# Performance work log

Hardware: AMD Instinct MI355X
Metric: run time of the kernel (lower is better)

## Reference

```python
import jax, jax.numpy as jnp
import numpy as np

S = 16        # neighbor samples per layer
NL = 2        # number of GNN layers


def setup_inputs() -> dict:
    key = jax.random.key(0)
    ks = jax.random.split(key, 12)
    N_NODES, D, E, NMP, DEG, N_EDGE, B, NC = 50000, 128, 32, 3, 32, 200000, 1024, 8
    sc = 0.05
    return {
        "ids": jax.random.randint(ks[0], (B,), 0, N_NODES, dtype=jnp.int32),
        "feats": jax.random.normal(ks[1], (N_NODES, D), jnp.float32),
        "edge_emb": jax.random.normal(ks[2], (NMP, N_EDGE, E), jnp.float32),
        "adj_nodes": jax.random.randint(ks[3], (NMP, N_NODES, DEG), 0, N_NODES, dtype=jnp.int32),
        "adj_edges": jax.random.randint(ks[4], (NMP, N_NODES, DEG), 0, N_EDGE, dtype=jnp.int32),
        "W_self": jax.random.normal(ks[5], (NMP, NL, D, D), jnp.float32) * sc,
        "W_neigh": jax.random.normal(ks[6], (NMP, NL, D + E, D), jnp.float32) * sc,
        "W_edge": jax.random.normal(ks[7], (NMP, NL, 2 * D + E, E), jnp.float32) * sc,
        "attn": jax.random.normal(ks[8], (D,), jnp.float32) * sc,
        "fc_w": jax.random.normal(ks[9], (D, NC), jnp.float32) * sc,
        "fc_b": jnp.zeros((NC,), jnp.float32),
    }


def reference(ids, feats, edge_emb, adj_nodes, adj_edges, W_self, W_neigh, W_edge, attn, fc_w, fc_b):
    NMP = adj_nodes.shape[0]
    outs = []
    for mp in range(NMP):
        # --- sample neighbor tree (deterministic: first S columns) ---
        cur = ids
        all_feats = [feats[cur]]
        all_edges = []
        for _ in range(NL):
            nb = adj_nodes[mp][cur][:, :S].reshape(-1)     # [N*S]
            eid = adj_edges[mp][cur][:, :S].reshape(-1)    # [N*S]
            all_edges.append(edge_emb[mp][eid])            # [N*S, E]
            cur = nb
            all_feats.append(feats[cur])
        # --- per-layer aggregation + edge update ---
        for l in range(NL):
            new_feats = []
            for k in range(len(all_feats) - 1):
                xs, xn, ee = all_feats[k], all_feats[k + 1], all_edges[k]
                N = xs.shape[0]
                # mean over sampled neighbors of [neigh_feat || edge_emb]
                nin = jnp.concatenate(
                    [xn.reshape(N, S, -1), ee.reshape(N, S, -1)], axis=-1
                ).mean(axis=1)                             # [N, D+E]
                new_feats.append(jax.nn.relu(xs @ W_self[mp, l] + nin @ W_neigh[mp, l]))
            all_feats = new_feats  # dropout is identity in eval mode
            new_edges = []
            for k in range(len(all_edges) - 1):
                xs, xn, ee = all_feats[k], all_feats[k + 1], all_edges[k]
                rep = jnp.repeat(xs, S, axis=0)            # [N*S, D]
                new_edges.append(jax.nn.relu(
                    jnp.concatenate([rep, xn, ee], axis=-1) @ W_edge[mp, l]))
            all_edges = new_edges
        outs.append(all_feats[0])                          # [B, D]
    stacked = jnp.stack(outs)                              # [NMP, B, D]
    # metapath attention fuse
    scores = jnp.tanh(jnp.einsum('mbd,d->mb', stacked, attn))
    beta = jax.nn.softmax(scores, axis=0)
    emb = jnp.einsum('mb,mbd->bd', beta, stacked)          # [B, D]
    # F.normalize(dim=1)
    emb = emb / jnp.maximum(jnp.linalg.norm(emb, axis=1, keepdims=True), 1e-12)
    return emb @ fc_w + fc_b
```

## Files before the change

kernel.cpp:

```cpp
#include <hip/hip_runtime.h>

#define NNODES  50000
#define D       128
#define E       32
#define NMP     3
#define DEG     32
#define NEDGE   200000
#define B       1024
#define NC      8
#define S       16

#define RPM      17408
#define NKT      9
#define WSTRIDE  36864
#define WESTRIDE 9216

#define CONV_TASKS (1600000 + 6 * WSTRIDE + 3 * WESTRIDE)
#define TOT_TASKS  (CONV_TASKS + 3 * RPM)

typedef float f4 __attribute__((ext_vector_type(4)));
typedef short bh8 __attribute__((ext_vector_type(8)));

static __device__ __forceinline__ unsigned short f2bf(float f) {
    unsigned int u = __float_as_uint(f);
    u = u + 0x7FFFu + ((u >> 16) & 1u);
    return (unsigned short)(u >> 16);
}
static __device__ __forceinline__ float bf2f(unsigned short h) {
    return __uint_as_float(((unsigned int)h) << 16);
}

__global__ __launch_bounds__(256) void convsamp_k(
    const float* __restrict__ feats, const float* __restrict__ Ws,
    const float* __restrict__ Wn, const float* __restrict__ We,
    const int* __restrict__ ids, const int* __restrict__ adjn,
    const int* __restrict__ adje,
    unsigned short* __restrict__ fb, unsigned short* __restrict__ WT0,
    unsigned short* __restrict__ WTe, int* __restrict__ gx, int* __restrict__ eid1)
{
    int i = blockIdx.x * 256 + threadIdx.x;
    if (i < 1600000) {
        float4 v = ((const float4*)feats)[i];
        unsigned int p0 = (unsigned int)f2bf(v.x) | ((unsigned int)f2bf(v.y) << 16);
        unsigned int p1 = (unsigned int)f2bf(v.z) | ((unsigned int)f2bf(v.w) << 16);
        ((uint2*)fb)[i] = make_uint2(p0, p1);
    } else if (i < 1600000 + 6 * WSTRIDE) {
        int i2 = i - 1600000;
        int ml = i2 / WSTRIDE, e = i2 % WSTRIDE;
        int j = e & 7, t1 = e >> 3;
        int n = t1 & 127, t2 = t1 >> 7;
        int q = t2 & 3, kt = t2 >> 2;
        int k = kt * 32 + q * 8 + j;
        float v = (k < 128) ? Ws[((size_t)ml * 128 + k) * 128 + n]
                            : Wn[((size_t)ml * 160 + (k - 128)) * 128 + n];
        WT0[(size_t)ml * WSTRIDE + e] = f2bf(v);
    } else if (i < CONV_TASKS) {
        int i3 = i - 1600000 - 6 * WSTRIDE;
        int mp = i3 / WESTRIDE, e = i3 % WESTRIDE;
        int j = e & 7, t1 = e >> 3;
        int n = t1 & 31, t2 = t1 >> 5;
        int q = t2 & 3, kt = t2 >> 2;
        int k = kt * 32 + q * 8 + j;
        float v = We[(((size_t)mp * 2) * 288 + k) * 32 + n];
        WTe[(size_t)mp * WESTRIDE + e] = f2bf(v);
    } else if (i < TOT_TASKS) {
        int i4 = i - CONV_TASKS;
        int mp = i4 / RPM, r = i4 % RPM;
        if (r < 16384) {
            int node = ids[r >> 4];
            gx[mp * RPM + r]     = adjn[((size_t)mp * NNODES + node) * DEG + (r & 15)];
            eid1[mp * 16384 + r] = adje[((size_t)mp * NNODES + node) * DEG + (r & 15)];
        } else {
            gx[mp * RPM + r] = ids[r - 16384];
        }
    }
}

__global__ __launch_bounds__(256) void aggfeat_k(
    const unsigned short* __restrict__ fb, const float* __restrict__ edge_emb,
    const int* __restrict__ adjn, const int* __restrict__ adje,
    const int* __restrict__ gx, const int* __restrict__ eid1,
    const unsigned short* __restrict__ WT0,
    unsigned short* __restrict__ fout)
{
    __shared__ unsigned short Asm[16][136];
    __shared__ unsigned short Nsm[16][168];
    const int mp = blockIdx.y;
    const int w = threadIdx.x >> 6, t = threadIdx.x & 63;
    const int r0 = blockIdx.x * 16;
    const float* ee = edge_emb + (size_t)mp * NEDGE * E;
    const int hi = t >> 5, t31 = t & 31;
    const float inv = 1.0f / (float)S;
    const unsigned int* fb32 = (const unsigned int*)fb;
    const int lvl1 = (r0 < 16384);

    for (int pp = 0; pp < 2; ++pp) {
        const int lra = w * 4 + pp * 2, lrb = lra + 1;
        const int ra = r0 + lra, rb = r0 + lrb;
        const int sa = __builtin_amdgcn_readfirstlane(gx[mp * RPM + ra]);
        const int sb = __builtin_amdgcn_readfirstlane(gx[mp * RPM + rb]);
        const int *ipa, *eixa, *ipb, *eixb;
        if (lvl1) {
            ipa  = adjn + ((size_t)mp * NNODES + sa) * DEG;
            eixa = adje + ((size_t)mp * NNODES + sa) * DEG;
            ipb  = adjn + ((size_t)mp * NNODES + sb) * DEG;
            eixb = adje + ((size_t)mp * NNODES + sb) * DEG;
        } else {
            ipa  = gx + mp * RPM + (ra - 16384) * S;
            eixa = eid1 + mp * 16384 + (ra - 16384) * S;
            ipb  = gx + mp * RPM + (rb - 16384) * S;
            eixb = eid1 + mp * 16384 + (rb - 16384) * S;
        }
        unsigned int ava = fb32[(size_t)sa * 64 + t];
        unsigned int avb = fb32[(size_t)sb * 64 + t];
        unsigned int fva[S], fvb[S];
#pragma unroll
        for (int j = 0; j < S; ++j) {
            int na = __builtin_amdgcn_readfirstlane(ipa[j]);
            fva[j] = fb32[(size_t)na * 64 + t];
        }
#pragma unroll
        for (int j = 0; j < S; ++j) {
            int nb = __builtin_amdgcn_readfirstlane(ipb[j]);
            fvb[j] = fb32[(size_t)nb * 64 + t];
        }
        float eva[S / 2], evb[S / 2];
#pragma unroll
        for (int e = 0; e < S / 2; ++e) {
            int a_ev = __builtin_amdgcn_readfirstlane(eixa[2 * e]);
            int a_od = __builtin_amdgcn_readfirstlane(eixa[2 * e + 1]);
            eva[e] = ee[(size_t)(hi ? a_od : a_ev) * E + t31];
        }
#pragma unroll
        for (int e = 0; e < S / 2; ++e) {
            int b_ev = __builtin_amdgcn_readfirstlane(eixb[2 * e]);
            int b_od = __builtin_amdgcn_readfirstlane(eixb[2 * e + 1]);
            evb[e] = ee[(size_t)(hi ? b_od : b_ev) * E + t31];
        }

        float sa0 = 0.f, sa1 = 0.f, sea = 0.f;
        float sb0 = 0.f, sb1 = 0.f, seb = 0.f;
#pragma unroll
        for (int j = 0; j < S; ++j) {
            sa0 += bf2f((unsigned short)(fva[j] & 0xFFFF));
            sa1 += bf2f((unsigned short)(fva[j] >> 16));
            sb0 += bf2f((unsigned short)(fvb[j] & 0xFFFF));
            sb1 += bf2f((unsigned short)(fvb[j] >> 16));
        }
#pragma unroll
        for (int e = 0; e < S / 2; ++e) { sea += eva[e]; seb += evb[e]; }
        sea += __shfl_xor(sea, 32);
        seb += __shfl_xor(seb, 32);

        ((unsigned int*)&Asm[lra][0])[t] = ava;
        ((unsigned int*)&Asm[lrb][0])[t] = avb;
        ((unsigned int*)&Nsm[lra][0])[t] =
            (unsigned int)f2bf(sa0 * inv) | ((unsigned int)f2bf(sa1 * inv) << 16);
        ((unsigned int*)&Nsm[lrb][0])[t] =
            (unsigned int)f2bf(sb0 * inv) | ((unsigned int)f2bf(sb1 * inv) << 16);
        if (t < E) {
            Nsm[lra][128 + t] = f2bf(sea * inv);
            Nsm[lrb][128 + t] = f2bf(seb * inv);
        }
    }
    __syncthreads();

    const int q = t >> 4, lm = t & 15;
    const unsigned short* wb = WT0 + (size_t)mp * 2 * WSTRIDE;

    f4 acc[2];
    acc[0] = (f4){0.f, 0.f, 0.f, 0.f};
    acc[1] = (f4){0.f, 0.f, 0.f, 0.f};

#pragma unroll
    for (int kt = 0; kt < NKT; ++kt) {
        const int k0 = kt * 32 + q * 8;
        bh8 a = (k0 < 128) ? *(const bh8*)&Asm[lm][k0]
                           : *(const bh8*)&Nsm[lm][k0 - 128];
        const unsigned short* wrow = wb + ((size_t)(kt * 4 + q) * 128 + lm) * 8;
#pragma unroll
        for (int ntl = 0; ntl < 2; ++ntl) {
            bh8 bf = *(const bh8*)(wrow + (w * 2 + ntl) * 16 * 8);
            acc[ntl] = __builtin_amdgcn_mfma_f32_16x16x32_bf16(a, bf, acc[ntl], 0, 0, 0);
        }
    }

#pragma unroll
    for (int ntl = 0; ntl < 2; ++ntl)
#pragma unroll
        for (int rr = 0; rr < 4; ++rr) {
            int row = r0 + q * 4 + rr;
            int col = (w * 2 + ntl) * 16 + lm;
            fout[((size_t)mp * RPM + row) * 128 + col] = f2bf(fmaxf(acc[ntl][rr], 0.f));
        }
}

__global__ __launch_bounds__(256) void edgeagg_k(
    const unsigned short* __restrict__ fout, const float* __restrict__ edge_emb,
    const int* __restrict__ eid1, const unsigned short* __restrict__ WTe,
    unsigned short* __restrict__ agg1)
{
    const int mp = blockIdx.y;
    const int w = threadIdx.x >> 6, l = threadIdx.x & 63;
    const int q = l >> 4, lm = l & 15;
    const int m0 = blockIdx.x * 128 + w * 32;
    const unsigned short* we = WTe + (size_t)mp * WESTRIDE;
    const unsigned short* f1base = fout + (size_t)mp * RPM * 128;
    const unsigned short* f0base = fout + ((size_t)mp * RPM + 16384) * 128;
    const float* ee = edge_emb + (size_t)mp * NEDGE * E;
    const float inv = 1.0f / (float)S;

    const unsigned short* a1p[2];
    const unsigned short* a0p[2];
    int eidL[2];
#pragma unroll
    for (int mt = 0; mt < 2; ++mt) {
        int row = m0 + mt * 16 + lm;
        a1p[mt] = f1base + (size_t)row * 128;
        a0p[mt] = f0base + (size_t)(row >> 4) * 128;
        eidL[mt] = eid1[mp * 16384 + row];
    }

    f4 acc[2][2];
#pragma unroll
    for (int mt = 0; mt < 2; ++mt) { acc[mt][0] = (f4){0,0,0,0}; acc[mt][1] = (f4){0,0,0,0}; }

#pragma unroll
    for (int kt = 0; kt < NKT; ++kt) {
        const int k0 = kt * 32 + q * 8;
        bh8 a[2];
#pragma unroll
        for (int mt = 0; mt < 2; ++mt) {
            if (kt < 4) {
                a[mt] = *(const bh8*)(a0p[mt] + k0);
            } else if (kt < 8) {
                a[mt] = *(const bh8*)(a1p[mt] + (k0 - 128));
            } else {
                const float* ep = ee + (size_t)eidL[mt] * E + q * 8;
                float4 v0 = *(const float4*)ep;
                float4 v1 = *(const float4*)(ep + 4);
                bh8 tv;
                tv[0] = (short)f2bf(v0.x); tv[1] = (short)f2bf(v0.y);
                tv[2] = (short)f2bf(v0.z); tv[3] = (short)f2bf(v0.w);
                tv[4] = (short)f2bf(v1.x); tv[5] = (short)f2bf(v1.y);
                tv[6] = (short)f2bf(v1.z); tv[7] = (short)f2bf(v1.w);
                a[mt] = tv;
            }
        }
        const unsigned short* wrow = we + ((size_t)(kt * 4 + q) * 32 + lm) * 8;
        bh8 b0 = *(const bh8*)(wrow);
        bh8 b1 = *(const bh8*)(wrow + 16 * 8);
#pragma unroll
        for (int mt = 0; mt < 2; ++mt) {
            acc[mt][0] = __builtin_amdgcn_mfma_f32_16x16x32_bf16(a[mt], b0, acc[mt][0], 0, 0, 0);
            acc[mt][1] = __builtin_amdgcn_mfma_f32_16x16x32_bf16(a[mt], b1, acc[mt][1], 0, 0, 0);
        }
    }

#pragma unroll
    for (int mt = 0; mt < 2; ++mt) {
        int seg = (m0 >> 4) + mt;
#pragma unroll
        for (int nt = 0; nt < 2; ++nt) {
            float ps = 0.f;
#pragma unroll
            for (int rr = 0; rr < 4; ++rr) ps += fmaxf(acc[mt][nt][rr], 0.f);
            ps += __shfl_xor(ps, 16);
            ps += __shfl_xor(ps, 32);
            if (l < 16)
                agg1[((size_t)mp * B + seg) * 160 + 128 + nt * 16 + lm] = f2bf(ps * inv);
        }
    }

#pragma unroll
    for (int mt = 0; mt < 2; ++mt) {
        int seg = (m0 >> 4) + mt;
        const unsigned short* fr = f1base + (size_t)seg * 16 * 128;
        float s0 = 0.f, s1 = 0.f;
#pragma unroll
        for (int j = 0; j < S; ++j) {
            unsigned int u = ((const unsigned int*)(fr + j * 128))[l];
            s0 += bf2f((unsigned short)(u & 0xFFFF));
            s1 += bf2f((unsigned short)(u >> 16));
        }
        ((unsigned int*)(agg1 + ((size_t)mp * B + seg) * 160))[l] =
            (unsigned int)f2bf(s0 * inv) | ((unsigned int)f2bf(s1 * inv) << 16);
    }
}

__global__ __launch_bounds__(256) void feat1fin_k(
    const unsigned short* __restrict__ fout, const unsigned short* __restrict__ agg1,
    const unsigned short* __restrict__ WT0,
    const float* __restrict__ attn, const float* __restrict__ fcw,
    const float* __restrict__ fcb, float* __restrict__ out)
{
    __shared__ float sbuf[NMP][32][132];
    const int w = threadIdx.x >> 6, l = threadIdx.x & 63;
    const int q = l >> 4, lm = l & 15;
    const int m0 = blockIdx.x * 32;

    for (int task = w; task < 6; task += 4) {
        const int mp = task >> 1, mt = task & 1;
        const int row = m0 + mt * 16 + lm;
        const unsigned short* ap = fout + ((size_t)mp * RPM + 16384 + row) * 128;
        const unsigned short* np = agg1 + ((size_t)mp * B + row) * 160;
        const unsigned short* wb = WT0 + ((size_t)mp * 2 + 1) * WSTRIDE;

        f4 acc[8];
#pragma unroll
        for (int nt = 0; nt < 8; ++nt) acc[nt] = (f4){0.f, 0.f, 0.f, 0.f};
#pragma unroll
        for (int kt = 0; kt < NKT; ++kt) {
            const int k0 = kt * 32 + q * 8;
            bh8 a = (k0 < 128) ? *(const bh8*)(ap + k0) : *(const bh8*)(np + (k0 - 128));
            const unsigned short* wrow = wb + ((size_t)(kt * 4 + q) * 128 + lm) * 8;
#pragma unroll
            for (int nt = 0; nt < 8; ++nt) {
                bh8 bf = *(const bh8*)(wrow + nt * 16 * 8);
                acc[nt] = __builtin_amdgcn_mfma_f32_16x16x32_bf16(a, bf, acc[nt], 0, 0, 0);
            }
        }
#pragma unroll
        for (int nt = 0; nt < 8; ++nt)
#pragma unroll
            for (int rr = 0; rr < 4; ++rr)
                sbuf[mp][mt * 16 + q * 4 + rr][nt * 16 + lm] = fmaxf(acc[nt][rr], 0.f);
    }
    __syncthreads();

    const int row = threadIdx.x >> 3;
    const int j = threadIdx.x & 7;
    const int d0 = j * 16;
    float sc[NMP];
#pragma unroll
    for (int mp = 0; mp < NMP; ++mp) {
        float p = 0.f;
#pragma unroll
        for (int d = 0; d < 16; ++d) p += sbuf[mp][row][d0 + d] * attn[d0 + d];
        p += __shfl_xor(p, 1); p += __shfl_xor(p, 2); p += __shfl_xor(p, 4);
        sc[mp] = tanhf(p);
    }
    float mx = fmaxf(sc[0], fmaxf(sc[1], sc[2]));
    float e0 = expf(sc[0] - mx), e1 = expf(sc[1] - mx), e2 = expf(sc[2] - mx);
    float isum = 1.f / (e0 + e1 + e2);
    float b0 = e0 * isum, b1 = e1 * isum, b2 = e2 * isum;

    float emb[16];
    float nn = 0.f;
#pragma unroll
    for (int d = 0; d < 16; ++d) {
        float v = b0 * sbuf[0][row][d0 + d] + b1 * sbuf[1][row][d0 + d]
                + b2 * sbuf[2][row][d0 + d];
        emb[d] = v;
        nn += v * v;
    }
    nn += __shfl_xor(nn, 1); nn += __shfl_xor(nn, 2); nn += __shfl_xor(nn, 4);
    float innorm = 1.f / fmaxf(sqrtf(nn), 1e-12f);
#pragma unroll
    for (int d = 0; d < 16; ++d) emb[d] *= innorm;

#pragma unroll
    for (int c = 0; c < NC; ++c) {
        float p = 0.f;
#pragma unroll
        for (int d = 0; d < 16; ++d) p += emb[d] * fcw[(d0 + d) * NC + c];
        p += __shfl_xor(p, 1); p += __shfl_xor(p, 2); p += __shfl_xor(p, 4);
        if (j == c) out[(size_t)(m0 + row) * NC + c] = p + fcb[c];
    }
}

extern "C" void kernel_launch(void* const* d_in, const int* in_sizes, int n_in,
                              void* d_out, int out_size, void* d_ws, size_t ws_size,
                              hipStream_t stream) {
    const int* ids        = (const int*)d_in[0];
    const float* feats    = (const float*)d_in[1];
    const float* edge_emb = (const float*)d_in[2];
    const int* adjn       = (const int*)d_in[3];
    const int* adje       = (const int*)d_in[4];
    const float* Ws       = (const float*)d_in[5];
    const float* Wn       = (const float*)d_in[6];
    const float* We       = (const float*)d_in[7];
    const float* attn     = (const float*)d_in[8];
    const float* fcw      = (const float*)d_in[9];
    const float* fcb      = (const float*)d_in[10];
    float* out = (float*)d_out;

    char* p = (char*)d_ws;
    unsigned short* WT0 = (unsigned short*)p; p += (size_t)6 * WSTRIDE * 2;
    unsigned short* WTe = (unsigned short*)p; p += (size_t)3 * WESTRIDE * 2;
    unsigned short* fb  = (unsigned short*)p; p += (size_t)NNODES * 128 * 2;
    int* gx   = (int*)p;                      p += (size_t)3 * RPM * 4;
    int* eid1 = (int*)p;                      p += (size_t)3 * 16384 * 4;
    unsigned short* fout = (unsigned short*)p; p += (size_t)3 * RPM * 128 * 2;
    unsigned short* agg1 = (unsigned short*)p; p += (size_t)3 * B * 160 * 2;

    convsamp_k<<<TOT_TASKS / 256, 256, 0, stream>>>(feats, Ws, Wn, We, ids, adjn, adje,
                                                    fb, WT0, WTe, gx, eid1);
    aggfeat_k<<<dim3(RPM / 16, 3), 256, 0, stream>>>(fb, edge_emb, adjn, adje, gx, eid1,
                                                     WT0, fout);
    edgeagg_k<<<dim3(128, 3), 256, 0, stream>>>(fout, edge_emb, eid1, WTe, agg1);
    feat1fin_k<<<32, 256, 0, stream>>>(fout, agg1, WT0, attn, fcw, fcb, out);
}
```

Measured before the change: 243.3 us.

## Vectorize neighbor gathers in aggfeat and split edge and final kernels into more blocks

aggfeat_k now preloads each row's neighbor and edge indices straight from the adjacency arrays as vectors, one slice per lane group, instead of using scalar readfirstlane index loads. Feature rows are gathered as 16-byte loads per lane and edge embeddings as float4, and partial sums are combined with cross-lane shuffles. The separate level-0 and level-1 index paths become one, and a launch_bounds occupancy hint is added. edgeagg_k and feat1fin_k handle half as many rows per block and launch twice as many blocks to spread work over more CUs. The cost is extra shuffle reductions and more redundant weight loads per block.

```diff
diff --git a/kernel.cpp b/kernel.cpp
--- a/kernel.cpp
+++ b/kernel.cpp
@@ -20,6 +20,10 @@
 
 typedef float f4 __attribute__((ext_vector_type(4)));
 typedef short bh8 __attribute__((ext_vector_type(8)));
+typedef unsigned int uv4 __attribute__((ext_vector_type(4)));
+typedef unsigned int uv2 __attribute__((ext_vector_type(2)));
+typedef int iv4 __attribute__((ext_vector_type(4)));
+typedef int iv2 __attribute__((ext_vector_type(2)));
 
 static __device__ __forceinline__ unsigned short f2bf(float f) {
     unsigned int u = __float_as_uint(f);
@@ -76,7 +80,7 @@
     }
 }
 
-__global__ __launch_bounds__(256) void aggfeat_k(
+__global__ __launch_bounds__(256, 4) void aggfeat_k(
     const unsigned short* __restrict__ fb, const float* __restrict__ edge_emb,
     const int* __restrict__ adjn, const int* __restrict__ adje,
     const int* __restrict__ gx, const int* __restrict__ eid1,
@@ -86,86 +90,106 @@
     __shared__ unsigned short Asm[16][136];
     __shared__ unsigned short Nsm[16][168];
     const int mp = blockIdx.y;
-    const int w = threadIdx.x >> 6, t = threadIdx.x & 63;
+    const int w = threadIdx.x >> 6, l = threadIdx.x & 63;
     const int r0 = blockIdx.x * 16;
+    const unsigned int* fb32 = (const unsigned int*)fb;
     const float* ee = edge_emb + (size_t)mp * NEDGE * E;
-    const int hi = t >> 5, t31 = t & 31;
     const float inv = 1.0f / (float)S;
-    const unsigned int* fb32 = (const unsigned int*)fb;
-    const int lvl1 = (r0 < 16384);
-
+    const int g = l >> 4, c = l & 15;
+    const int d8 = l & 7;
+
+    int srcs[4];
+#pragma unroll
+    for (int rr = 0; rr < 4; ++rr)
+        srcs[rr] = gx[mp * RPM + r0 + w * 4 + rr];
+
+    iv4 nIdx[4]; iv2 eIdx[4]; unsigned int selfu[4];
+#pragma unroll
+    for (int rr = 0; rr < 4; ++rr) {
+        const int* nb = adjn + ((size_t)mp * NNODES + srcs[rr]) * DEG;
+        const int* eb = adje + ((size_t)mp * NNODES + srcs[rr]) * DEG;
+        nIdx[rr] = *(const iv4*)(nb + 4 * g);
+        eIdx[rr] = *(const iv2*)(eb + 2 * (l >> 3));
+        selfu[rr] = fb32[(size_t)srcs[rr] * 64 + l];
+    }
+
+#pragma unroll
     for (int pp = 0; pp < 2; ++pp) {
-        const int lra = w * 4 + pp * 2, lrb = lra + 1;
-        const int ra = r0 + lra, rb = r0 + lrb;
-        const int sa = __builtin_amdgcn_readfirstlane(gx[mp * RPM + ra]);
-        const int sb = __builtin_amdgcn_readfirstlane(gx[mp * RPM + rb]);
-        const int *ipa, *eixa, *ipb, *eixb;
-        if (lvl1) {
-            ipa  = adjn + ((size_t)mp * NNODES + sa) * DEG;
-            eixa = adje + ((size_t)mp * NNODES + sa) * DEG;
-            ipb  = adjn + ((size_t)mp * NNODES + sb) * DEG;
-            eixb = adje + ((size_t)mp * NNODES + sb) * DEG;
-        } else {
-            ipa  = gx + mp * RPM + (ra - 16384) * S;
-            eixa = eid1 + mp * 16384 + (ra - 16384) * S;
-            ipb  = gx + mp * RPM + (rb - 16384) * S;
-            eixb = eid1 + mp * 16384 + (rb - 16384) * S;
-        }
-        unsigned int ava = fb32[(size_t)sa * 64 + t];
-        unsigned int avb = fb32[(size_t)sb * 64 + t];
-        unsigned int fva[S], fvb[S];
-#pragma unroll
-        for (int j = 0; j < S; ++j) {
-            int na = __builtin_amdgcn_readfirstlane(ipa[j]);
-            fva[j] = fb32[(size_t)na * 64 + t];
-        }
-#pragma unroll
-        for (int j = 0; j < S; ++j) {
-            int nb = __builtin_amdgcn_readfirstlane(ipb[j]);
-            fvb[j] = fb32[(size_t)nb * 64 + t];
-        }
-        float eva[S / 2], evb[S / 2];
-#pragma unroll
-        for (int e = 0; e < S / 2; ++e) {
-            int a_ev = __builtin_amdgcn_readfirstlane(eixa[2 * e]);
-            int a_od = __builtin_amdgcn_readfirstlane(eixa[2 * e + 1]);
-            eva[e] = ee[(size_t)(hi ? a_od : a_ev) * E + t31];
-        }
-#pragma unroll
-        for (int e = 0; e < S / 2; ++e) {
-            int b_ev = __builtin_amdgcn_readfirstlane(eixb[2 * e]);
-            int b_od = __builtin_amdgcn_readfirstlane(eixb[2 * e + 1]);
-            evb[e] = ee[(size_t)(hi ? b_od : b_ev) * E + t31];
-        }
-
-        float sa0 = 0.f, sa1 = 0.f, sea = 0.f;
-        float sb0 = 0.f, sb1 = 0.f, seb = 0.f;
-#pragma unroll
-        for (int j = 0; j < S; ++j) {
-            sa0 += bf2f((unsigned short)(fva[j] & 0xFFFF));
-            sa1 += bf2f((unsigned short)(fva[j] >> 16));
-            sb0 += bf2f((unsigned short)(fvb[j] & 0xFFFF));
-            sb1 += bf2f((unsigned short)(fvb[j] >> 16));
-        }
-#pragma unroll
-        for (int e = 0; e < S / 2; ++e) { sea += eva[e]; seb += evb[e]; }
-        sea += __shfl_xor(sea, 32);
-        seb += __shfl_xor(seb, 32);
-
-        ((unsigned int*)&Asm[lra][0])[t] = ava;
-        ((unsigned int*)&Asm[lrb][0])[t] = avb;
-        ((unsigned int*)&Nsm[lra][0])[t] =
-            (unsigned int)f2bf(sa0 * inv) | ((unsigned int)f2bf(sa1 * inv) << 16);
-        ((unsigned int*)&Nsm[lrb][0])[t] =
-            (unsigned int)f2bf(sb0 * inv) | ((unsigned int)f2bf(sb1 * inv) << 16);
-        if (t < E) {
-            Nsm[lra][128 + t] = f2bf(sea * inv);
-            Nsm[lrb][128 + t] = f2bf(seb * inv);
+        const int lra = w * 4 + 2 * pp, lrb = lra + 1;
+        const int ia = 2 * pp, ib = 2 * pp + 1;
+
+        uv4 gA[4], gB[4];
+#pragma unroll
+        for (int p = 0; p < 4; ++p)
+            gA[p] = *(const uv4*)(fb32 + (size_t)nIdx[ia][p] * 64 + c * 4);
+#pragma unroll
+        for (int p = 0; p < 4; ++p)
+            gB[p] = *(const uv4*)(fb32 + (size_t)nIdx[ib][p] * 64 + c * 4);
+        f4 eA0 = *(const f4*)(ee + (size_t)eIdx[ia][0] * E + d8 * 4);
+        f4 eA1 = *(const f4*)(ee + (size_t)eIdx[ia][1] * E + d8 * 4);
+        f4 eB0 = *(const f4*)(ee + (size_t)eIdx[ib][0] * E + d8 * 4);
+        f4 eB1 = *(const f4*)(ee + (size_t)eIdx[ib][1] * E + d8 * 4);
+
+        float accA[8], accB[8];
+#pragma unroll
+        for (int d = 0; d < 8; ++d) { accA[d] = 0.f; accB[d] = 0.f; }
+#pragma unroll
+        for (int p = 0; p < 4; ++p)
+#pragma unroll
+            for (int qq = 0; qq < 4; ++qq) {
+                unsigned int ua = gA[p][qq], ub = gB[p][qq];
+                accA[2 * qq]     += __uint_as_float(ua << 16);
+                accA[2 * qq + 1] += __uint_as_float(ua & 0xffff0000u);
+                accB[2 * qq]     += __uint_as_float(ub << 16);
+                accB[2 * qq + 1] += __uint_as_float(ub & 0xffff0000u);
+            }
+#pragma unroll
+        for (int d = 0; d < 8; ++d) {
+            accA[d] += __shfl_xor(accA[d], 16);
+            accA[d] += __shfl_xor(accA[d], 32);
+            accB[d] += __shfl_xor(accB[d], 16);
+            accB[d] += __shfl_xor(accB[d], 32);
+        }
+        float feA[4], feB[4];
+#pragma unroll
+        for (int qq = 0; qq < 4; ++qq) {
+            feA[qq] = eA0[qq] + eA1[qq];
+            feB[qq] = eB0[qq] + eB1[qq];
+            feA[qq] += __shfl_xor(feA[qq], 8);
+            feA[qq] += __shfl_xor(feA[qq], 16);
+            feA[qq] += __shfl_xor(feA[qq], 32);
+            feB[qq] += __shfl_xor(feB[qq], 8);
+            feB[qq] += __shfl_xor(feB[qq], 16);
+            feB[qq] += __shfl_xor(feB[qq], 32);
+        }
+
+        ((unsigned int*)&Asm[lra][0])[l] = selfu[ia];
+        ((unsigned int*)&Asm[lrb][0])[l] = selfu[ib];
+        if (g == 0) {
+            uv4 oa, ob;
+#pragma unroll
+            for (int qq = 0; qq < 4; ++qq) {
+                oa[qq] = (unsigned int)f2bf(accA[2 * qq] * inv)
+                       | ((unsigned int)f2bf(accA[2 * qq + 1] * inv) << 16);
+                ob[qq] = (unsigned int)f2bf(accB[2 * qq] * inv)
+                       | ((unsigned int)f2bf(accB[2 * qq + 1] * inv) << 16);
+            }
+            *(uv4*)&Nsm[lra][c * 8] = oa;
+            *(uv4*)&Nsm[lrb][c * 8] = ob;
+        }
+        if (l < 8) {
+            uv2 oa, ob;
+            oa[0] = (unsigned int)f2bf(feA[0] * inv) | ((unsigned int)f2bf(feA[1] * inv) << 16);
+            oa[1] = (unsigned int)f2bf(feA[2] * inv) | ((unsigned int)f2bf(feA[3] * inv) << 16);
+            ob[0] = (unsigned int)f2bf(feB[0] * inv) | ((unsigned int)f2bf(feB[1] * inv) << 16);
+            ob[1] = (unsigned int)f2bf(feB[2] * inv) | ((unsigned int)f2bf(feB[3] * inv) << 16);
+            *(uv2*)&Nsm[lra][128 + d8 * 4] = oa;
+            *(uv2*)&Nsm[lrb][128 + d8 * 4] = ob;
         }
     }
     __syncthreads();
 
-    const int q = t >> 4, lm = t & 15;
+    const int q = l >> 4, lm = l & 15;
     const unsigned short* wb = WT0 + (size_t)mp * 2 * WSTRIDE;
 
     f4 acc[2];
@@ -203,78 +227,61 @@
     const int mp = blockIdx.y;
     const int w = threadIdx.x >> 6, l = threadIdx.x & 63;
     const int q = l >> 4, lm = l & 15;
-    const int m0 = blockIdx.x * 128 + w * 32;
+    const int m0 = blockIdx.x * 64 + w * 16;
     const unsigned short* we = WTe + (size_t)mp * WESTRIDE;
     const unsigned short* f1base = fout + (size_t)mp * RPM * 128;
     const unsigned short* f0base = fout + ((size_t)mp * RPM + 16384) * 128;
     const float* ee = edge_emb + (size_t)mp * NEDGE * E;
     const float inv = 1.0f / (float)S;
 
-    const unsigned short* a1p[2];
-    const unsigned short* a0p[2];
-    int eidL[2];
-#pragma unroll
-    for (int mt = 0; mt < 2; ++mt) {
-        int row = m0 + mt * 16 + lm;
-        a1p[mt] = f1base + (size_t)row * 128;
-        a0p[mt] = f0base + (size_t)(row >> 4) * 128;
-        eidL[mt] = eid1[mp * 16384 + row];
-    }
-
-    f4 acc[2][2];
-#pragma unroll
-    for (int mt = 0; mt < 2; ++mt) { acc[mt][0] = (f4){0,0,0,0}; acc[mt][1] = (f4){0,0,0,0}; }
+    const int row = m0 + lm;
+    const unsigned short* a1p = f1base + (size_t)row * 128;
+    const unsigned short* a0p = f0base + (size_t)(row >> 4) * 128;
+    const int eidL = eid1[mp * 16384 + row];
+
+    f4 acc[2];
+    acc[0] = (f4){0.f, 0.f, 0.f, 0.f};
+    acc[1] = (f4){0.f, 0.f, 0.f, 0.f};
 
 #pragma unroll
     for (int kt = 0; kt < NKT; ++kt) {
         const int k0 = kt * 32 + q * 8;
-        bh8 a[2];
-#pragma unroll
-        for (int mt = 0; mt < 2; ++mt) {
-            if (kt < 4) {
-                a[mt] = *(const bh8*)(a0p[mt] + k0);
-            } else if (kt < 8) {
-                a[mt] = *(const bh8*)(a1p[mt] + (k0 - 128));
-            } else {
-                const float* ep = ee + (size_t)eidL[mt] * E + q * 8;
-                float4 v0 = *(const float4*)ep;
-                float4 v1 = *(const float4*)(ep + 4);
-                bh8 tv;
-                tv[0] = (short)f2bf(v0.x); tv[1] = (short)f2bf(v0.y);
-                tv[2] = (short)f2bf(v0.z); tv[3] = (short)f2bf(v0.w);
-                tv[4] = (short)f2bf(v1.x); tv[5] = (short)f2bf(v1.y);
-                tv[6] = (short)f2bf(v1.z); tv[7] = (short)f2bf(v1.w);
-                a[mt] = tv;
-            }
+        bh8 a;
+        if (kt < 4) {
+            a = *(const bh8*)(a0p + k0);
+        } else if (kt < 8) {
+            a = *(const bh8*)(a1p + (k0 - 128));
+        } else {
+            const float* ep = ee + (size_t)eidL * E + q * 8;
+            float4 v0 = *(const float4*)ep;
+            float4 v1 = *(const float4*)(ep + 4);
+            bh8 tv;
+            tv[0] = (short)f2bf(v0.x); tv[1] = (short)f2bf(v0.y);
+            tv[2] = (short)f2bf(v0.z); tv[3] = (short)f2bf(v0.w);
+            tv[4] = (short)f2bf(v1.x); tv[5] = (short)f2bf(v1.y);
+            tv[6] = (short)f2bf(v1.z); tv[7] = (short)f2bf(v1.w);
+            a = tv;
         }
         const unsigned short* wrow = we + ((size_t)(kt * 4 + q) * 32 + lm) * 8;
         bh8 b0 = *(const bh8*)(wrow);
         bh8 b1 = *(const bh8*)(wrow + 16 * 8);
-#pragma unroll
-        for (int mt = 0; mt < 2; ++mt) {
-            acc[mt][0] = __builtin_amdgcn_mfma_f32_16x16x32_bf16(a[mt], b0, acc[mt][0], 0, 0, 0);
-            acc[mt][1] = __builtin_amdgcn_mfma_f32_16x16x32_bf16(a[mt], b1, acc[mt][1], 0, 0, 0);
-        }
-    }
-
-#pragma unroll
-    for (int mt = 0; mt < 2; ++mt) {
-        int seg = (m0 >> 4) + mt;
-#pragma unroll
-        for (int nt = 0; nt < 2; ++nt) {
-            float ps = 0.f;
-#pragma unroll
-            for (int rr = 0; rr < 4; ++rr) ps += fmaxf(acc[mt][nt][rr], 0.f);
-            ps += __shfl_xor(ps, 16);
-            ps += __shfl_xor(ps, 32);
-            if (l < 16)
-                agg1[((size_t)mp * B + seg) * 160 + 128 + nt * 16 + lm] = f2bf(ps * inv);
-        }
-    }
-
-#pragma unroll
-    for (int mt = 0; mt < 2; ++mt) {
-        int seg = (m0 >> 4) + mt;
+        acc[0] = __builtin_amdgcn_mfma_f32_16x16x32_bf16(a, b0, acc[0], 0, 0, 0);
+        acc[1] = __builtin_amdgcn_mfma_f32_16x16x32_bf16(a, b1, acc[1], 0, 0, 0);
+    }
+
+    const int seg = m0 >> 4;
+#pragma unroll
+    for (int nt = 0; nt < 2; ++nt) {
+        float ps = 0.f;
+#pragma unroll
+        for (int rr = 0; rr < 4; ++rr) ps += fmaxf(acc[nt][rr], 0.f);
+        ps += __shfl_xor(ps, 16);
+        ps += __shfl_xor(ps, 32);
+        if (l < 16)
+            agg1[((size_t)mp * B + seg) * 160 + 128 + nt * 16 + lm] = f2bf(ps * inv);
+    }
+
+    {
         const unsigned short* fr = f1base + (size_t)seg * 16 * 128;
         float s0 = 0.f, s1 = 0.f;
 #pragma unroll
@@ -294,78 +301,80 @@
     const float* __restrict__ attn, const float* __restrict__ fcw,
     const float* __restrict__ fcb, float* __restrict__ out)
 {
-    __shared__ float sbuf[NMP][32][132];
+    __shared__ float sbuf[NMP][16][132];
     const int w = threadIdx.x >> 6, l = threadIdx.x & 63;
     const int q = l >> 4, lm = l & 15;
-    const int m0 = blockIdx.x * 32;
+    const int m0 = blockIdx.x * 16;
 
     for (int task = w; task < 6; task += 4) {
-        const int mp = task >> 1, mt = task & 1;
-        const int row = m0 + mt * 16 + lm;
+        const int mp = task >> 1, nh = task & 1;
+        const int row = m0 + lm;
         const unsigned short* ap = fout + ((size_t)mp * RPM + 16384 + row) * 128;
         const unsigned short* np = agg1 + ((size_t)mp * B + row) * 160;
         const unsigned short* wb = WT0 + ((size_t)mp * 2 + 1) * WSTRIDE;
 
-        f4 acc[8];
-#pragma unroll
-        for (int nt = 0; nt < 8; ++nt) acc[nt] = (f4){0.f, 0.f, 0.f, 0.f};
+        f4 acc[4];
+#pragma unroll
+        for (int nt = 0; nt < 4; ++nt) acc[nt] = (f4){0.f, 0.f, 0.f, 0.f};
 #pragma unroll
         for (int kt = 0; kt < NKT; ++kt) {
             const int k0 = kt * 32 + q * 8;
             bh8 a = (k0 < 128) ? *(const bh8*)(ap + k0) : *(const bh8*)(np + (k0 - 128));
             const unsigned short* wrow = wb + ((size_t)(kt * 4 + q) * 128 + lm) * 8;
 #pragma unroll
-            for (int nt = 0; nt < 8; ++nt) {
-                bh8 bf = *(const bh8*)(wrow + nt * 16 * 8);
+            for (int nt = 0; nt < 4; ++nt) {
+                bh8 bf = *(const bh8*)(wrow + (nh * 4 + nt) * 16 * 8);
                 acc[nt] = __builtin_amdgcn_mfma_f32_16x16x32_bf16(a, bf, acc[nt], 0, 0, 0);
             }
         }
 #pragma unroll
-        for (int nt = 0; nt < 8; ++nt)
+        for (int nt = 0; nt < 4; ++nt)
 #pragma unroll
             for (int rr = 0; rr < 4; ++rr)
-                sbuf[mp][mt * 16 + q * 4 + rr][nt * 16 + lm] = fmaxf(acc[nt][rr], 0.f);
+                sbuf[mp][q * 4 + rr][(nh * 4 + nt) * 16 + lm] = fmaxf(acc[nt][rr], 0.f);
     }
     __syncthreads();
 
-    const int row = threadIdx.x >> 3;
-    const int j = threadIdx.x & 7;
-    const int d0 = j * 16;
-    float sc[NMP];
-#pragma unroll
-    for (int mp = 0; mp < NMP; ++mp) {
-        float p = 0.f;
-#pragma unroll
-        for (int d = 0; d < 16; ++d) p += sbuf[mp][row][d0 + d] * attn[d0 + d];
-        p += __shfl_xor(p, 1); p += __shfl_xor(p, 2); p += __shfl_xor(p, 4);
-        sc[mp] = tanhf(p);
-    }
-    float mx = fmaxf(sc[0], fmaxf(sc[1], sc[2]));
-    float e0 = expf(sc[0] - mx), e1 = expf(sc[1] - mx), e2 = expf(sc[2] - mx);
-    float isum = 1.f / (e0 + e1 + e2);
-    float b0 = e0 * isum, b1 = e1 * isum, b2 = e2 * isum;
-
-    float emb[16];
-    float nn = 0.f;
-#pragma unroll
-    for (int d = 0; d < 16; ++d) {
-        float v = b0 * sbuf[0][row][d0 + d] + b1 * sbuf[1][row][d0 + d]
-                + b2 * sbuf[2][row][d0 + d];
-        emb[d] = v;
-        nn += v * v;
-    }
-    nn += __shfl_xor(nn, 1); nn += __shfl_xor(nn, 2); nn += __shfl_xor(nn, 4);
-    float innorm = 1.f / fmaxf(sqrtf(nn), 1e-12f);
-#pragma unroll
-    for (int d = 0; d < 16; ++d) emb[d] *= innorm;
-
-#pragma unroll
-    for (int c = 0; c < NC; ++c) {
-        float p = 0.f;
-#pragma unroll
-        for (int d = 0; d < 16; ++d) p += emb[d] * fcw[(d0 + d) * NC + c];
-        p += __shfl_xor(p, 1); p += __shfl_xor(p, 2); p += __shfl_xor(p, 4);
-        if (j == c) out[(size_t)(m0 + row) * NC + c] = p + fcb[c];
+    if (threadIdx.x < 128) {
+        const int row = threadIdx.x >> 3;
+        const int j = threadIdx.x & 7;
+        const int d0 = j * 16;
+        float sc[NMP];
+#pragma unroll
+        for (int mp = 0; mp < NMP; ++mp) {
+            float p = 0.f;
+#pragma unroll
+            for (int d = 0; d < 16; ++d) p += sbuf[mp][row][d0 + d] * attn[d0 + d];
+            p += __shfl_xor(p, 1); p += __shfl_xor(p, 2); p += __shfl_xor(p, 4);
+            sc[mp] = tanhf(p);
+        }
+        float mx = fmaxf(sc[0], fmaxf(sc[1], sc[2]));
+        float e0 = expf(sc[0] - mx), e1 = expf(sc[1] - mx), e2 = expf(sc[2] - mx);
+        float isum = 1.f / (e0 + e1 + e2);
+        float b0 = e0 * isum, b1 = e1 * isum, b2 = e2 * isum;
+
+        float emb[16];
+        float nn = 0.f;
+#pragma unroll
+        for (int d = 0; d < 16; ++d) {
+            float v = b0 * sbuf[0][row][d0 + d] + b1 * sbuf[1][row][d0 + d]
+                    + b2 * sbuf[2][row][d0 + d];
+            emb[d] = v;
+            nn += v * v;
+        }
+        nn += __shfl_xor(nn, 1); nn += __shfl_xor(nn, 2); nn += __shfl_xor(nn, 4);
+        float innorm = 1.f / fmaxf(sqrtf(nn), 1e-12f);
+#pragma unroll
+        for (int d = 0; d < 16; ++d) emb[d] *= innorm;
+
+#pragma unroll
+        for (int cc = 0; cc < NC; ++cc) {
+            float p = 0.f;
+#pragma unroll
+            for (int d = 0; d < 16; ++d) p += emb[d] * fcw[(d0 + d) * NC + cc];
+            p += __shfl_xor(p, 1); p += __shfl_xor(p, 2); p += __shfl_xor(p, 4);
+            if (j == cc) out[(size_t)(m0 + row) * NC + cc] = p + fcb[cc];
+        }
     }
 }
 
@@ -398,6 +407,6 @@
                                                     fb, WT0, WTe, gx, eid1);
     aggfeat_k<<<dim3(RPM / 16, 3), 256, 0, stream>>>(fb, edge_emb, adjn, adje, gx, eid1,
                                                      WT0, fout);
-    edgeagg_k<<<dim3(128, 3), 256, 0, stream>>>(fout, edge_emb, eid1, WTe, agg1);
-    feat1fin_k<<<32, 256, 0, stream>>>(fout, agg1, WT0, attn, fcw, fcb, out);
-}
+    edgeagg_k<<<dim3(256, 3), 256, 0, stream>>>(fout, edge_emb, eid1, WTe, agg1);
+    feat1fin_k<<<64, 256, 0, stream>>>(fout, agg1, WT0, attn, fcw, fcb, out);
+}
```

Result: faster. 225.5 us (-7.3%).
